# Performance work log

Hardware: AMD Instinct MI355X
Metric: run time of the kernel (lower is better)

## Reference

```python
import jax, jax.numpy as jnp
import numpy as np

B, K, DIM, T_FRAMES = 4, 200, 256, 800

def _conv1d_same(x, w, b):
    # x: [B, K, Cin], w: [3, Cin, Cout] (WIO), 'same' padding over token axis
    y = jax.lax.conv_general_dilated(x, w, window_strides=(1,), padding='SAME',
                                     dimension_numbers=('NWC', 'WIO', 'NWC'))
    return y + b

def _swish_block(x, w1, b1, w2, b2):
    x = jax.nn.silu(x @ w1 + b1)
    return jax.nn.silu(x @ w2 + b2)

def setup_inputs() -> dict:
    key = jax.random.key(0)
    ks = jax.random.split(key, 10)
    def lin(k, fan_in, shape):
        return jax.random.normal(k, shape, dtype=jnp.float32) / np.sqrt(fan_in)
    inp = {
        'T': T_FRAMES,
        'durations': jax.random.uniform(ks[0], (B, K), dtype=jnp.float32) * 4.0,
        'features': jax.random.normal(ks[1], (B, K, DIM), dtype=jnp.float32),
        'conv1_w': lin(ks[2], 3 * DIM, (3, DIM, 8)),
        'conv1_b': jnp.zeros((8,), jnp.float32),
        'conv2_w': lin(ks[3], 3 * DIM, (3, DIM, 8)),
        'conv2_b': jnp.zeros((8,), jnp.float32),
        'sw1_w1': lin(ks[4], 10, (10, 16)), 'sw1_b1': jnp.zeros((16,), jnp.float32),
        'sw1_w2': lin(ks[5], 16, (16, 16)), 'sw1_b2': jnp.zeros((16,), jnp.float32),
        'sw2_w1': lin(ks[6], 10, (10, 2)), 'sw2_b1': jnp.zeros((2,), jnp.float32),
        'sw2_w2': lin(ks[7], 2, (2, 2)), 'sw2_b2': jnp.zeros((2,), jnp.float32),
        'p1_w': lin(ks[8], 2, (2, 1)), 'p1_b': jnp.zeros((1,), jnp.float32),
        'p2_w': lin(ks[9], 16, (16, DIM)), 'p2_b': jnp.zeros((DIM,), jnp.float32),
    }
    return inp

def reference(T, durations, features, conv1_w, conv1_b, conv2_w, conv2_b,
              sw1_w1, sw1_b1, sw1_w2, sw1_b2, sw2_w1, sw2_b1, sw2_w2, sw2_b2,
              p1_w, p1_b, p2_w, p2_b):
    # Conv + SiLU token feature extraction: [B, K, 8]
    left = jax.nn.silu(_conv1d_same(features, conv1_w, conv1_b))
    right = jax.nn.silu(_conv1d_same(features, conv2_w, conv2_b))
    # Token boundary grids S, E: [B, T, K]
    token_end = jnp.cumsum(durations, axis=1)          # [B, K]
    token_start = token_end - durations                # [B, K]
    t = jnp.arange(T, dtype=features.dtype)            # frame index grid
    S = t[None, :, None] - token_start[:, None, :]     # [B, T, K]
    E = token_end[:, None, :] - t[None, :, None]       # [B, T, K]
    Bn, Tn, Kn = S.shape
    # Concat (S, E, conv_feats) -> [B, T, K, 10]
    xleft = jnp.concatenate([S[..., None], E[..., None],
                             jnp.broadcast_to(left[:, None], (Bn, Tn, Kn, 8))], axis=-1)
    xright = jnp.concatenate([S[..., None], E[..., None],
                              jnp.broadcast_to(right[:, None], (Bn, Tn, Kn, 8))], axis=-1)
    C = _swish_block(xleft, sw1_w1, sw1_b1, sw1_w2, sw1_b2)      # [B, T, K, 16]
    r = _swish_block(xright, sw2_w1, sw2_b1, sw2_w2, sw2_b2)     # [B, T, K, 2]
    logits = (r @ p1_w + p1_b)[..., 0]                           # [B, T, K]
    W = jax.nn.softmax(logits, axis=-1)                          # attention over tokens
    # Upsampled output: weighted token features + projected auxiliary context
    O = jnp.einsum('btk,bkd->btd', W, features)
    A = jnp.einsum('btk,btkp->btp', W, C)                        # [B, T, 16]
    return O + (A @ p2_w + p2_b)
```

## Files before the change

### kernel.cpp

```cpp
#include <hip/hip_runtime.h>
#include <math.h>

#define B_   4
#define K_   200
#define DIM_ 256
#define T_   800

#define S_UP 68
#define CW_R 20

__device__ __forceinline__ float silu_f(float x) {
    return x * __builtin_amdgcn_rcpf(1.0f + __expf(-x));
}

__global__ __launch_bounds__(256) void prep_kernel(
        const float* __restrict__ dur,
        const float* __restrict__ feats,
        const float* __restrict__ c1w, const float* __restrict__ c1b,
        const float* __restrict__ c2w, const float* __restrict__ c2b,
        const float* __restrict__ sw1_w1, const float* __restrict__ sw1_b1,
        const float* __restrict__ sw1_w2,
        const float* __restrict__ sw2_w1, const float* __restrict__ sw2_b1,
        float* __restrict__ cw) {
    const int b = blockIdx.y, k0 = blockIdx.x * 4;
    const int tid = threadIdx.x, w = tid >> 6, l = tid & 63;

    __shared__ float wT[16][772];
    __shared__ float red[64][S_UP];
    __shared__ float sSc[K_], sEc[K_];
    __shared__ float sfeat[4][16];

    if (blockIdx.x == 0 && blockIdx.y == 0) {
        cw[(size_t)B_ * K_ * CW_R + tid] = sw1_w2[((tid & 15) * 16) + (tid >> 4)];
    }

    for (int i = tid; i < 3 * DIM_ * 8; i += 256) {
        int tc = i >> 3, o = i & 7;
        wT[o][tc]     = c1w[i];
        wT[8 + o][tc] = c2w[i];
    }
    if (tid < 64) {
        float4 dv = make_float4(0.f, 0.f, 0.f, 0.f);
        if (tid < 50) dv = *(const float4*)&dur[b * K_ + tid * 4];
        float s0 = dv.x, s1 = s0 + dv.y, s2 = s1 + dv.z, s3 = s2 + dv.w;
        float sc = s3;
#pragma unroll
        for (int off = 1; off < 64; off <<= 1) {
            float v = __shfl_up(sc, off);
            if (tid >= off) sc += v;
        }
        float excl = sc - s3;
        if (tid < 50) {
            *(float4*)&sSc[tid * 4] = make_float4(excl, excl + s0, excl + s1, excl + s2);
            *(float4*)&sEc[tid * 4] = make_float4(excl + s0, excl + s1, excl + s2, excl + s3);
        }
    }
    __syncthreads();

    {
        const int k = k0 + w;
        const float4* f4 = (const float4*)feats;
        float4 fv[3];
#pragma unroll
        for (int tap = 0; tap < 3; ++tap) {
            int kk = k - 1 + tap;
            bool valid = (kk >= 0 && kk < K_);
            int kc = valid ? kk : 0;
            float4 v = f4[(size_t)(b * K_ + kc) * 64 + l];
            fv[tap] = valid ? v : make_float4(0.f, 0.f, 0.f, 0.f);
        }
        float acc[16];
#pragma unroll
        for (int oc = 0; oc < 16; ++oc) acc[oc] = 0.f;
#pragma unroll
        for (int tap = 0; tap < 3; ++tap) {
#pragma unroll
            for (int oc = 0; oc < 16; ++oc) {
                float4 wv = *(const float4*)&wT[oc][tap * DIM_ + 4 * l];
                acc[oc] += fv[tap].x * wv.x + fv[tap].y * wv.y
                         + fv[tap].z * wv.z + fv[tap].w * wv.w;
            }
        }
#pragma unroll
        for (int oc = 0; oc < 16; ++oc) red[w * 16 + oc][l] = acc[oc];
    }
    __syncthreads();
    {
        const int rwv = tid >> 6, oc = (tid >> 2) & 15, rq = tid & 3;
        const float* base = &red[rwv * 16 + oc][rq * 16];
        float4 b0 = *(const float4*)&base[0];
        float4 b1 = *(const float4*)&base[4];
        float4 b2 = *(const float4*)&base[8];
        float4 b3 = *(const float4*)&base[12];
        float s = b0.x + b0.y + b0.z + b0.w + b1.x + b1.y + b1.z + b1.w
                + b2.x + b2.y + b2.z + b2.w + b3.x + b3.y + b3.z + b3.w;
        s += __shfl_down(s, 1);
        s += __shfl_down(s, 2);
        if (rq == 0) {
            float bias = (oc < 8) ? c1b[oc] : c2b[oc & 7];
            sfeat[rwv][oc] = silu_f(s + bias);
        }
    }
    __syncthreads();

    if (tid < 64) {
        const int j = tid >> 2, klc = tid & 3, kk = k0 + klc;
        float st = sSc[kk], en = sEc[kk];
        float a = sw1_b1[j] - st * sw1_w1[j] + en * sw1_w1[16 + j];
#pragma unroll
        for (int i = 0; i < 8; ++i) a += sfeat[klc][i] * sw1_w1[(2 + i) * 16 + j];
        cw[(size_t)(b * K_ + kk) * CW_R + 2 + j] = a;
    } else if (tid < 72) {
        const int idx = tid - 64, which = idx >> 2, klc = idx & 3, kk = k0 + klc;
        float st = sSc[kk], en = sEc[kk];
        float a = sw2_b1[which] - st * sw2_w1[which] + en * sw2_w1[2 + which];
#pragma unroll
        for (int i = 0; i < 8; ++i) a += sfeat[klc][8 + i] * sw2_w1[(2 + i) * 2 + which];
        cw[(size_t)(b * K_ + kk) * CW_R + which] = a;
    }
}

__global__ __launch_bounds__(256, 4) void main_kernel(
        const float* __restrict__ feats,
        const float* __restrict__ cw,
        const float* __restrict__ sw1_w1, const float* __restrict__ sw1_b2,
        const float* __restrict__ sw2_w1, const float* __restrict__ sw2_w2,
        const float* __restrict__ sw2_b2,
        const float* __restrict__ p1_w,   const float* __restrict__ p1_b,
        const float* __restrict__ p2_w,   const float* __restrict__ p2_b,
        float* __restrict__ out) {
    const int t0 = blockIdx.x * 4, b = blockIdx.y;
    const int tid = threadIdx.x, w = tid >> 6, l = tid & 63;
    const int t = t0 + w;

    __shared__ alignas(16) float apool[64 * S_UP];
    __shared__ alignas(16) float opool[16 * 256];
    __shared__ alignas(16) float W4[K_][4];
    __shared__ alignas(16) float At[16][4];

    const float* __restrict__ w2T = cw + (size_t)B_ * K_ * CW_R;

    const float* cbg = cw + (size_t)b * K_ * CW_R;
    int kc[4];
#pragma unroll
    for (int i = 0; i < 4; ++i) { int k = l + 64 * i; kc[i] = (k < K_) ? k : (K_ - 1); }

    const float tf = (float)t;
    float ajt[16];
#pragma unroll
    for (int j = 0; j < 16; ++j) ajt[j] = (sw1_w1[j] - sw1_w1[16 + j]) * tf;

    float c0[4], c1[4], hmat[4][16];
#pragma unroll
    for (int i = 0; i < 4; ++i) {
        const float* base = cbg + (size_t)kc[i] * CW_R;
        float r[20];
#pragma unroll
        for (int q = 0; q < 5; ++q) *(float4*)&r[4 * q] = *(const float4*)(base + 4 * q);
        c0[i] = r[0]; c1[i] = r[1];
#pragma unroll
        for (int j = 0; j < 16; ++j) hmat[i][j] = silu_f(ajt[j] + r[2 + j]);
    }

    const float a0 = sw2_w1[0] - sw2_w1[2], a1 = sw2_w1[1] - sw2_w1[3];
    const float rw20 = sw2_w2[0], rw21 = sw2_w2[1], rw22 = sw2_w2[2], rw23 = sw2_w2[3];
    const float rb20 = sw2_b2[0], rb21 = sw2_b2[1];
    const float p10 = p1_w[0], p11 = p1_w[1], p1b0 = p1_b[0];

    float lg[4];
#pragma unroll
    for (int i = 0; i < 4; ++i) {
        float h0 = silu_f(fmaf(a0, tf, c0[i]));
        float h1 = silu_f(fmaf(a1, tf, c1[i]));
        float g0 = silu_f(rb20 + h0 * rw20 + h1 * rw22);
        float g1 = silu_f(rb21 + h0 * rw21 + h1 * rw23);
        lg[i] = (l + 64 * i < K_) ? (g0 * p10 + g1 * p11 + p1b0) : -1e30f;
    }
    float m = fmaxf(fmaxf(lg[0], lg[1]), fmaxf(lg[2], lg[3]));
#pragma unroll
    for (int off = 32; off > 0; off >>= 1) m = fmaxf(m, __shfl_xor(m, off));
    float e0 = __expf(lg[0] - m), e1 = __expf(lg[1] - m);
    float e2 = __expf(lg[2] - m), e3 = __expf(lg[3] - m);
    float ssum = e0 + e1 + e2 + e3;
#pragma unroll
    for (int off = 32; off > 0; off >>= 1) ssum += __shfl_xor(ssum, off);
    float inv = __builtin_amdgcn_rcpf(ssum);
    float wgt[4] = { e0 * inv, e1 * inv, e2 * inv, e3 * inv };
#pragma unroll
    for (int i = 0; i < 4; ++i) { int k = l + 64 * i; if (k < K_) W4[k][w] = wgt[i]; }

    float acc[16];
#pragma unroll
    for (int j = 0; j < 16; ++j) {
        const float* __restrict__ wj = w2T + j * 16;
        const float bj = sw1_b2[j];
        float s = 0.f;
#pragma unroll
        for (int i = 0; i < 4; ++i) {
            float c = bj;
#pragma unroll
            for (int p = 0; p < 16; ++p) c += hmat[i][p] * wj[p];
            s += wgt[i] * silu_f(c);
        }
        acc[j] = s;
    }
#pragma unroll
    for (int j = 0; j < 16; ++j) apool[(w * 16 + j) * S_UP + l] = acc[j];

    const int kb = w * 50;
    const float4* fB4 = (const float4*)(feats + (size_t)b * K_ * DIM_);
    float4 pf[8];
#pragma unroll
    for (int q = 0; q < 8; ++q) pf[q] = fB4[(size_t)(kb + q) * 64 + l];

    __syncthreads();

    {
        const int rwv = tid >> 6, rj = (tid >> 2) & 15, rq = tid & 3;
        const float* base = &apool[(rwv * 16 + rj) * S_UP + rq * 16];
        float4 b0 = *(const float4*)&base[0];
        float4 b1 = *(const float4*)&base[4];
        float4 b2 = *(const float4*)&base[8];
        float4 b3 = *(const float4*)&base[12];
        float s = b0.x + b0.y + b0.z + b0.w + b1.x + b1.y + b1.z + b1.w
                + b2.x + b2.y + b2.z + b2.w + b3.x + b3.y + b3.z + b3.w;
        s += __shfl_down(s, 1);
        s += __shfl_down(s, 2);
        if (rq == 0) At[rj][rwv] = s;
    }

    {
        float4 po[4];
#pragma unroll
        for (int f = 0; f < 4; ++f) po[f] = make_float4(0.f, 0.f, 0.f, 0.f);
#pragma unroll
        for (int kk = 0; kk < 8; ++kk) {
            float4 wv = *(const float4*)&W4[kb + kk][0];
            float4 fv = pf[kk];
            po[0].x += wv.x * fv.x; po[0].y += wv.x * fv.y; po[0].z += wv.x * fv.z; po[0].w += wv.x * fv.w;
            po[1].x += wv.y * fv.x; po[1].y += wv.y * fv.y; po[1].z += wv.y * fv.z; po[1].w += wv.y * fv.w;
            po[2].x += wv.z * fv.x; po[2].y += wv.z * fv.y; po[2].z += wv.z * fv.z; po[2].w += wv.z * fv.w;
            po[3].x += wv.w * fv.x; po[3].y += wv.w * fv.y; po[3].z += wv.w * fv.z; po[3].w += wv.w * fv.w;
        }
#pragma unroll 6
        for (int kk = 8; kk < 50; ++kk) {
            float4 wv = *(const float4*)&W4[kb + kk][0];
            float4 fv = fB4[(size_t)(kb + kk) * 64 + l];
            po[0].x += wv.x * fv.x; po[0].y += wv.x * fv.y; po[0].z += wv.x * fv.z; po[0].w += wv.x * fv.w;
            po[1].x += wv.y * fv.x; po[1].y += wv.y * fv.y; po[1].z += wv.y * fv.z; po[1].w += wv.y * fv.w;
            po[2].x += wv.z * fv.x; po[2].y += wv.z * fv.y; po[2].z += wv.z * fv.z; po[2].w += wv.z * fv.w;
            po[3].x += wv.w * fv.x; po[3].y += wv.w * fv.y; po[3].z += wv.w * fv.z; po[3].w += wv.w * fv.w;
        }
#pragma unroll
        for (int f = 0; f < 4; ++f)
            *(float4*)&opool[((w * 4 + f) * 64 + l) * 4] = po[f];
    }
    __syncthreads();

    {
        const int f = tid >> 6, d4 = (tid & 63) * 4;
        float4 v = make_float4(0.f, 0.f, 0.f, 0.f);
#pragma unroll
        for (int ww = 0; ww < 4; ++ww) {
            float4 pv = *(const float4*)&opool[(ww * 4 + f) * 256 + d4];
            v.x += pv.x; v.y += pv.y; v.z += pv.z; v.w += pv.w;
        }
        float4 ab = *(const float4*)&p2_b[d4];
        v.x += ab.x; v.y += ab.y; v.z += ab.z; v.w += ab.w;
#pragma unroll
        for (int p = 0; p < 16; ++p) {
            float4 pw = *(const float4*)&p2_w[p * DIM_ + d4];
            float a = At[p][f];
            v.x += a * pw.x; v.y += a * pw.y; v.z += a * pw.z; v.w += a * pw.w;
        }
        *(float4*)&out[((size_t)b * T_ + t0 + f) * DIM_ + d4] = v;
    }
}

extern "C" void kernel_launch(void* const* d_in, const int* in_sizes, int n_in,
                              void* d_out, int out_size, void* d_ws, size_t ws_size,
                              hipStream_t stream) {
    const float* durations = (const float*)d_in[1];
    const float* features  = (const float*)d_in[2];
    const float* conv1_w   = (const float*)d_in[3];
    const float* conv1_b   = (const float*)d_in[4];
    const float* conv2_w   = (const float*)d_in[5];
    const float* conv2_b   = (const float*)d_in[6];
    const float* sw1_w1    = (const float*)d_in[7];
    const float* sw1_b1    = (const float*)d_in[8];
    const float* sw1_w2    = (const float*)d_in[9];
    const float* sw1_b2    = (const float*)d_in[10];
    const float* sw2_w1    = (const float*)d_in[11];
    const float* sw2_b1    = (const float*)d_in[12];
    const float* sw2_w2    = (const float*)d_in[13];
    const float* sw2_b2    = (const float*)d_in[14];
    const float* p1_w      = (const float*)d_in[15];
    const float* p1_b      = (const float*)d_in[16];
    const float* p2_w      = (const float*)d_in[17];
    const float* p2_b      = (const float*)d_in[18];
    float* out = (float*)d_out;

    float* cw = (float*)d_ws;

    prep_kernel<<<dim3(50, B_), 256, 0, stream>>>(
        durations, features, conv1_w, conv1_b, conv2_w, conv2_b,
        sw1_w1, sw1_b1, sw1_w2, sw2_w1, sw2_b1, cw);
    main_kernel<<<dim3(T_ / 4, B_), 256, 0, stream>>>(
        features, cw,
        sw1_w1, sw1_b2,
        sw2_w1, sw2_w2, sw2_b2,
        p1_w, p1_b, p2_w, p2_b, out);
}
```

Before: 119.8 us.

## Cut registers and LDS in main kernel to raise occupancy

Computes the first-layer hidden activations two tokens at a time instead of keeping all four 16-wide rows live, which lowers register pressure. The two shared-memory scratch buffers are merged into one aliased pool, with an extra barrier so the reduction reads finish before the buffer is reused. The launch bound goes from 4 to 5 waves per SIMD. The extra barrier and the recomputed per-token weight terms add some overhead, and a tighter register budget could cause spills.

```diff
diff --git a/kernel.cpp b/kernel.cpp
--- a/kernel.cpp
+++ b/kernel.cpp
@@ -120,7 +120,7 @@
     }
 }
 
-__global__ __launch_bounds__(256, 4) void main_kernel(
+__global__ __launch_bounds__(256, 5) void main_kernel(
         const float* __restrict__ feats,
         const float* __restrict__ cw,
         const float* __restrict__ sw1_w1, const float* __restrict__ sw1_b2,
@@ -133,10 +133,9 @@
     const int tid = threadIdx.x, w = tid >> 6, l = tid & 63;
     const int t = t0 + w;
 
-    __shared__ alignas(16) float apool[64 * S_UP];
-    __shared__ alignas(16) float opool[16 * 256];
+    __shared__ alignas(16) float pool[64 * S_UP];
     __shared__ alignas(16) float W4[K_][4];
-    __shared__ alignas(16) float At[16][4];
+    __shared__ alignas(16) float AtT[4][16];
 
     const float* __restrict__ w2T = cw + (size_t)B_ * K_ * CW_R;
 
@@ -146,20 +145,12 @@
     for (int i = 0; i < 4; ++i) { int k = l + 64 * i; kc[i] = (k < K_) ? k : (K_ - 1); }
 
     const float tf = (float)t;
-    float ajt[16];
-#pragma unroll
-    for (int j = 0; j < 16; ++j) ajt[j] = (sw1_w1[j] - sw1_w1[16 + j]) * tf;
-
-    float c0[4], c1[4], hmat[4][16];
+
+    float c0[4], c1[4];
 #pragma unroll
     for (int i = 0; i < 4; ++i) {
-        const float* base = cbg + (size_t)kc[i] * CW_R;
-        float r[20];
-#pragma unroll
-        for (int q = 0; q < 5; ++q) *(float4*)&r[4 * q] = *(const float4*)(base + 4 * q);
-        c0[i] = r[0]; c1[i] = r[1];
-#pragma unroll
-        for (int j = 0; j < 16; ++j) hmat[i][j] = silu_f(ajt[j] + r[2 + j]);
+        float4 h = *(const float4*)(cbg + (size_t)kc[i] * CW_R);
+        c0[i] = h.x; c1[i] = h.y;
     }
 
     const float a0 = sw2_w1[0] - sw2_w1[2], a1 = sw2_w1[1] - sw2_w1[3];
@@ -191,21 +182,39 @@
 
     float acc[16];
 #pragma unroll
-    for (int j = 0; j < 16; ++j) {
-        const float* __restrict__ wj = w2T + j * 16;
-        const float bj = sw1_b2[j];
-        float s = 0.f;
-#pragma unroll
-        for (int i = 0; i < 4; ++i) {
-            float c = bj;
-#pragma unroll
-            for (int p = 0; p < 16; ++p) c += hmat[i][p] * wj[p];
-            s += wgt[i] * silu_f(c);
-        }
-        acc[j] = s;
-    }
-#pragma unroll
-    for (int j = 0; j < 16; ++j) apool[(w * 16 + j) * S_UP + l] = acc[j];
+    for (int j = 0; j < 16; ++j) acc[j] = 0.f;
+#pragma unroll
+    for (int half = 0; half < 2; ++half) {
+        float hm[2][16];
+#pragma unroll
+        for (int ii = 0; ii < 2; ++ii) {
+            const int i = half * 2 + ii;
+            const float* base = cbg + (size_t)kc[i] * CW_R;
+            float r[20];
+#pragma unroll
+            for (int q = 0; q < 5; ++q)
+                *(float4*)&r[4 * q] = *(const float4*)(base + 4 * q);
+#pragma unroll
+            for (int j = 0; j < 16; ++j) {
+                float ajtj = (sw1_w1[j] - sw1_w1[16 + j]) * tf;
+                hm[ii][j] = silu_f(ajtj + r[2 + j]);
+            }
+        }
+#pragma unroll
+        for (int j = 0; j < 16; ++j) {
+            const float* __restrict__ wj = w2T + j * 16;
+            const float bj = sw1_b2[j];
+#pragma unroll
+            for (int ii = 0; ii < 2; ++ii) {
+                float c = bj;
+#pragma unroll
+                for (int p = 0; p < 16; ++p) c += hm[ii][p] * wj[p];
+                acc[j] += wgt[half * 2 + ii] * silu_f(c);
+            }
+        }
+    }
+#pragma unroll
+    for (int j = 0; j < 16; ++j) pool[(w * 16 + j) * S_UP + l] = acc[j];
 
     const int kb = w * 50;
     const float4* fB4 = (const float4*)(feats + (size_t)b * K_ * DIM_);
@@ -217,7 +226,7 @@
 
     {
         const int rwv = tid >> 6, rj = (tid >> 2) & 15, rq = tid & 3;
-        const float* base = &apool[(rwv * 16 + rj) * S_UP + rq * 16];
+        const float* base = &pool[(rwv * 16 + rj) * S_UP + rq * 16];
         float4 b0 = *(const float4*)&base[0];
         float4 b1 = *(const float4*)&base[4];
         float4 b2 = *(const float4*)&base[8];
@@ -226,8 +235,9 @@
                 + b2.x + b2.y + b2.z + b2.w + b3.x + b3.y + b3.z + b3.w;
         s += __shfl_down(s, 1);
         s += __shfl_down(s, 2);
-        if (rq == 0) At[rj][rwv] = s;
-    }
+        if (rq == 0) AtT[rwv][rj] = s;
+    }
+    __syncthreads();
 
     {
         float4 po[4];
@@ -253,7 +263,7 @@
         }
 #pragma unroll
         for (int f = 0; f < 4; ++f)
-            *(float4*)&opool[((w * 4 + f) * 64 + l) * 4] = po[f];
+            *(float4*)&pool[((w * 4 + f) * 64 + l) * 4] = po[f];
     }
     __syncthreads();
 
@@ -262,7 +272,7 @@
         float4 v = make_float4(0.f, 0.f, 0.f, 0.f);
 #pragma unroll
         for (int ww = 0; ww < 4; ++ww) {
-            float4 pv = *(const float4*)&opool[(ww * 4 + f) * 256 + d4];
+            float4 pv = *(const float4*)&pool[(ww * 4 + f) * 256 + d4];
             v.x += pv.x; v.y += pv.y; v.z += pv.z; v.w += pv.w;
         }
         float4 ab = *(const float4*)&p2_b[d4];
@@ -270,7 +280,7 @@
 #pragma unroll
         for (int p = 0; p < 16; ++p) {
             float4 pw = *(const float4*)&p2_w[p * DIM_ + d4];
-            float a = At[p][f];
+            float a = AtT[f][p];
             v.x += a * pw.x; v.y += a * pw.y; v.z += a * pw.z; v.w += a * pw.w;
         }
         *(float4*)&out[((size_t)b * T_ + t0 + f) * DIM_ + d4] = v;
```

New measurement: 124.7 us. 1.04x slower.
